# Kernel tuning notes

Measured on AMD Instinct MI355X. Metric: run time of the kernel, lower is better.

Reference implementation:

```python
import jax, jax.numpy as jnp
import numpy as np

N_NODES = 100000
N_EDGES = 1600000
IN_FEATS = 256
HIDDEN = 128
N_CLASSES = 128
NEG_SLOPE = 0.2


def setup_inputs() -> dict:
    key = jax.random.key(0)
    ks = jax.random.split(key, 12)
    inp = {
        "features": jax.random.normal(ks[0], (N_NODES, IN_FEATS), dtype=jnp.float32),
        "src": jax.random.randint(ks[1], (N_EDGES,), 0, N_NODES, dtype=jnp.int32),
        "dst": jax.random.randint(ks[2], (N_EDGES,), 0, N_NODES, dtype=jnp.int32),
        # layer 1 params (Xavier-ish scale)
        "W1": jax.random.normal(ks[3], (HIDDEN, IN_FEATS), dtype=jnp.float32) / np.sqrt(IN_FEATS),
        "al1": jax.random.normal(ks[4], (HIDDEN,), dtype=jnp.float32) / np.sqrt(HIDDEN),
        "ar1": jax.random.normal(ks[5], (HIDDEN,), dtype=jnp.float32) / np.sqrt(HIDDEN),
        "b1": jnp.zeros((HIDDEN,), dtype=jnp.float32),
        # layer 2 params
        "W2": jax.random.normal(ks[6], (N_CLASSES, HIDDEN), dtype=jnp.float32) / np.sqrt(HIDDEN),
        "al2": jax.random.normal(ks[7], (N_CLASSES,), dtype=jnp.float32) / np.sqrt(N_CLASSES),
        "ar2": jax.random.normal(ks[8], (N_CLASSES,), dtype=jnp.float32) / np.sqrt(N_CLASSES),
        "b2": jnp.zeros((N_CLASSES,), dtype=jnp.float32),
    }
    return inp


def _gat_conv(x, W, attn_l, attn_r, bias, src, dst):
    """Single-head DGL GATConv: fc -> edge leaky-relu scores -> segment softmax over dst -> scatter-sum."""
    h = x @ W.T                                   # [N, D]
    el = h @ attn_l                               # [N]
    er = h @ attn_r                               # [N]
    e = jax.nn.leaky_relu(el[src] + er[dst], NEG_SLOPE)   # [E]
    # numerically stable segment softmax over incoming edges of each dst node
    m = jax.ops.segment_max(e, dst, num_segments=N_NODES)          # [N] (-inf for empty)
    ex = jnp.exp(e - m[dst])                                       # [E]
    s = jax.ops.segment_sum(ex, dst, num_segments=N_NODES)         # [N]
    alpha = ex / s[dst]                                            # [E]
    out = jax.ops.segment_sum(h[src] * alpha[:, None], dst, num_segments=N_NODES)
    return out + bias


def reference(features, src, dst, W1, al1, ar1, b1, W2, al2, ar2, b2):
    x = _gat_conv(features, W1, al1, ar1, b1, src, dst)
    x = jax.nn.elu(x)
    return _gat_conv(x, W2, al2, ar2, b2, src, dst)
```

## Files before the change

kernel.cpp:

```cpp
#include <hip/hip_runtime.h>

typedef unsigned short u16;
typedef unsigned int u32;

#define NEG_SLOPE 0.2f

using short8 = __attribute__((ext_vector_type(8))) short;
using float4v = __attribute__((ext_vector_type(4))) float;

__device__ __forceinline__ float bfu(u16 v) { return __uint_as_float(((u32)v) << 16); }
__device__ __forceinline__ float bflo(u32 u) { return __uint_as_float(u << 16); }
__device__ __forceinline__ float bfhi(u32 u) { return __uint_as_float(u & 0xffff0000u); }
__device__ __forceinline__ u16 f2bf(float f) {
  u32 x = __float_as_uint(f);
  return (u16)((x + 0x7fffu + ((x >> 16) & 1u)) >> 16);
}
__device__ __forceinline__ float loadf(const void* p, int idx, int isbf) {
  return isbf ? bfu(((const u16*)p)[idx]) : ((const float*)p)[idx];
}

__global__ __launch_bounds__(256) void detect_dtype(const u32* __restrict__ w,
                                                    int nwords, int* __restrict__ flag) {
  __shared__ int cnt;
  if (threadIdx.x == 0) cnt = 0;
  __syncthreads();
  int c = 0;
  for (int i = threadIdx.x; i < nwords; i += 256) {
    u32 e = (w[i] >> 7) & 0xFFu;
    c += (e >= 0x60u && e <= 0x90u) ? 1 : 0;
  }
  atomicAdd(&cnt, c);
  __syncthreads();
  if (threadIdx.x == 0) flag[0] = (cnt * 2 > nwords) ? 1 : 0;
}

__global__ __launch_bounds__(256) void zero_i32(int* __restrict__ p, int n) {
  int i = blockIdx.x * 256 + threadIdx.x;
  if (i < n) p[i] = 0;
}


__global__ __launch_bounds__(256) void scan1(const int* __restrict__ counts,
                                             int* __restrict__ indptr,
                                             int* __restrict__ bsum, int N) {
  __shared__ int sh[256];
  int t = threadIdx.x;
  int idx = blockIdx.x * 256 + t;
  int v = (idx < N) ? counts[idx] : 0;
  sh[t] = v;
  __syncthreads();
  for (int off = 1; off < 256; off <<= 1) {
    int y = (t >= off) ? sh[t - off] : 0;
    __syncthreads();
    sh[t] += y;
    __syncthreads();
  }
  if (idx < N) indptr[idx] = sh[t] - v;
  if (t == 255) bsum[blockIdx.x] = sh[255];
}

__global__ __launch_bounds__(512) void scan2par(int* __restrict__ bsum, int NB) {
  __shared__ int sh[512];
  int t = threadIdx.x;
  int v = (t < NB) ? bsum[t] : 0;
  sh[t] = v;
  __syncthreads();
  for (int off = 1; off < 512; off <<= 1) {
    int y = (t >= off) ? sh[t - off] : 0;
    __syncthreads();
    sh[t] += y;
    __syncthreads();
  }
  if (t < NB) bsum[t] = sh[t] - v;
}

__global__ __launch_bounds__(256) void scan3(int* __restrict__ indptr,
                                             const int* __restrict__ boff,
                                             int N, int E) {
  int idx = blockIdx.x * 256 + threadIdx.x;
  if (idx < N) indptr[idx] += boff[blockIdx.x];
  if (idx == 0) indptr[N] = E;
}

__global__ __launch_bounds__(256) void scatter2(const int* __restrict__ src,
                                                const int* __restrict__ dst,
                                                const int* __restrict__ rank,
                                                const int* __restrict__ indptr,
                                                int* __restrict__ ssrc, int E) {
  int e = blockIdx.x * 256 + threadIdx.x;
  if (e < E) {
    int d = dst[e];
    ssrc[indptr[d] + rank[e]] = src[e];
  }
}

__global__ __launch_bounds__(256) void bsw_build(const void* __restrict__ W,
                                                 u16* __restrict__ Bsw, int K,
                                                 const int* __restrict__ dflag) {
  const int isbf = dflag[0];
  int t = blockIdx.x * 256 + threadIdx.x;
  int total = (K / 32) * 8 * 64;
  if (t >= total) return;
  int lane = t & 63;
  int c = (t >> 6) & 7;
  int ktile = t >> 9;
  int n = lane & 15, q = lane >> 4;
  int col = c * 16 + n;
  u16 vals[8];
#pragma unroll
  for (int j = 0; j < 8; ++j) {
    int k = ktile * 32 + q * 8 + j;
    int idx = col * K + k;
    vals[j] = isbf ? ((const u16*)W)[idx] : f2bf(((const float*)W)[idx]);
  }
  *(uint4*)(Bsw + (size_t)t * 8) = *(uint4*)vals;
}

template <int K, int DYNA>
__device__ __forceinline__ void gemm_body(int bix, const void* __restrict__ Xv,
                                          const u16* __restrict__ Bsw,
                                          u16* __restrict__ Hb,
                                          const void* __restrict__ al,
                                          const void* __restrict__ ar,
                                          float* __restrict__ el_,
                                          float* __restrict__ er_, int N,
                                          const int* __restrict__ dflag) {
  const int isbfP = dflag[0];
  const int isbfA = DYNA ? isbfP : 1;
  int tid = threadIdx.x;
  int w = tid >> 6, lane = tid & 63;
  int n = lane & 15, q = lane >> 4;
  int row0 = bix * 64 + w * 16;
  int m = row0 + n;
  int mclamp = (m < N) ? m : 0;

  float alv[8], arv[8];
#pragma unroll
  for (int c = 0; c < 8; ++c) {
    alv[c] = loadf(al, c * 16 + n, isbfP);
    arv[c] = loadf(ar, c * 16 + n, isbfP);
  }

  float4v acc[8];
#pragma unroll
  for (int c = 0; c < 8; ++c) acc[c] = (float4v){0.f, 0.f, 0.f, 0.f};

#pragma unroll
  for (int t = 0; t < K / 32; ++t) {
    short8 af;
    if (isbfA) {
      af = *(const short8*)((const u16*)Xv + (size_t)mclamp * K + t * 32 + q * 8);
    } else {
      const float* Af = (const float*)Xv + (size_t)mclamp * K + t * 32 + q * 8;
      float4 f0 = *(const float4*)Af;
      float4 f1 = *(const float4*)(Af + 4);
      u16 tmp[8] = {f2bf(f0.x), f2bf(f0.y), f2bf(f0.z), f2bf(f0.w),
                    f2bf(f1.x), f2bf(f1.y), f2bf(f1.z), f2bf(f1.w)};
      af = *(short8*)tmp;
    }
    const uint4* bt = (const uint4*)Bsw + ((size_t)t * 8) * 64 + lane;
#pragma unroll
    for (int c = 0; c < 8; ++c) {
      uint4 bw = bt[c * 64];
      short8 bf = *(short8*)&bw;
      acc[c] = __builtin_amdgcn_mfma_f32_16x16x32_bf16(af, bf, acc[c], 0, 0, 0);
    }
  }

#pragma unroll
  for (int c = 0; c < 8; ++c) {
#pragma unroll
    for (int r = 0; r < 4; ++r) {
      int row = row0 + q * 4 + r;
      if (row < N) Hb[(size_t)row * 128 + c * 16 + n] = f2bf(acc[c][r]);
    }
  }

#pragma unroll
  for (int r = 0; r < 4; ++r) {
    float sl = 0.f, sr = 0.f;
#pragma unroll
    for (int c = 0; c < 8; ++c) {
      float v = acc[c][r];
      sl = fmaf(v, alv[c], sl);
      sr = fmaf(v, arv[c], sr);
    }
#pragma unroll
    for (int off = 1; off < 16; off <<= 1) {
      sl += __shfl_xor(sl, off);
      sr += __shfl_xor(sr, off);
    }
    if (n == 0) {
      int row = row0 + q * 4 + r;
      if (row < N) {
        el_[row] = sl;
        er_[row] = sr;
      }
    }
  }
}

template <int K, int DYNA>
__global__ __launch_bounds__(256) void gemm_mfma(const void* __restrict__ Xv,
                                                 const u16* __restrict__ Bsw,
                                                 u16* __restrict__ Hb,
                                                 const void* __restrict__ al,
                                                 const void* __restrict__ ar,
                                                 float* __restrict__ el_,
                                                 float* __restrict__ er_, int N,
                                                 const int* __restrict__ dflag) {
  gemm_body<K, DYNA>(blockIdx.x, Xv, Bsw, Hb, al, ar, el_, er_, N, dflag);
}

template <int K, int DYNA>
__global__ __launch_bounds__(256) void fused_gemm_hist(
    const void* __restrict__ Xv, const u16* __restrict__ Bsw, u16* __restrict__ Hb,
    const void* __restrict__ al, const void* __restrict__ ar,
    float* __restrict__ el_, float* __restrict__ er_, int N,
    const int* __restrict__ dflag, int gemm_blocks,
    const int* __restrict__ dst, int* __restrict__ counts,
    int* __restrict__ rank, int E) {
  int bix = (int)blockIdx.x;
  if (bix < gemm_blocks) {
    gemm_body<K, DYNA>(bix, Xv, Bsw, Hb, al, ar, el_, er_, N, dflag);
  } else {
    int e = (bix - gemm_blocks) * 256 + threadIdx.x;
    if (e < E) rank[e] = atomicAdd(&counts[dst[e]], 1);
  }
}

template <int MODE>
__global__ __launch_bounds__(256) void agg_kernel(const u32* __restrict__ Hb,
                                                  const float* __restrict__ el,
                                                  const float* __restrict__ er,
                                                  const int* __restrict__ indptr,
                                                  const int* __restrict__ ssrc,
                                                  const void* __restrict__ bias,
                                                  void* __restrict__ outv, int N,
                                                  const int* __restrict__ dflag) {
  const int isbf = dflag[0];
  int tid = threadIdx.x;
  int n = blockIdx.x * 4 + (tid >> 6);
  int lane = tid & 63;
  if (n >= N) return;

  int beg = indptr[n];
  int end = indptr[n + 1];
  float ern = er[n];

  float ms[4], ll[4], aa0[4], aa1[4];
#pragma unroll
  for (int j = 0; j < 4; ++j) {
    ms[j] = -INFINITY; ll[j] = 0.f; aa0[j] = 0.f; aa1[j] = 0.f;
  }

  int p = beg;
  int id[8];
#pragma unroll
  for (int j = 0; j < 8; ++j) id[j] = (p + j < end) ? ssrc[p + j] : 0;
  float ev[4];
  u32 hv[4];
#pragma unroll
  for (int j = 0; j < 4; ++j) {
    ev[j] = el[id[j]];
    hv[j] = Hb[(size_t)id[j] * 64 + lane];
  }

  for (; p < end; p += 4) {
    float ev2[4];
    u32 hv2[4];
#pragma unroll
    for (int j = 0; j < 4; ++j) {
      ev2[j] = el[id[4 + j]];
      hv2[j] = Hb[(size_t)id[4 + j] * 64 + lane];
    }
    int idn[4];
#pragma unroll
    for (int j = 0; j < 4; ++j) idn[j] = (p + 8 + j < end) ? ssrc[p + 8 + j] : 0;

#pragma unroll
    for (int j = 0; j < 4; ++j) {
      if (p + j < end) {
        float sc = ev[j] + ern;
        sc = (sc > 0.f) ? sc : NEG_SLOPE * sc;
        float mn = fmaxf(ms[j], sc);
        float corr = __expf(ms[j] - mn), pe = __expf(sc - mn);
        ll[j] = ll[j] * corr + pe;
        aa0[j] = aa0[j] * corr + pe * bflo(hv[j]);
        aa1[j] = aa1[j] * corr + pe * bfhi(hv[j]);
        ms[j] = mn;
      }
    }
#pragma unroll
    for (int j = 0; j < 4; ++j) {
      id[j] = id[4 + j];
      id[4 + j] = idn[j];
      ev[j] = ev2[j];
      hv[j] = hv2[j];
    }
  }

  float mm = fmaxf(fmaxf(ms[0], ms[1]), fmaxf(ms[2], ms[3]));
  float msafe = (mm > -INFINITY) ? mm : 0.f;
  float l = 0.f, a0 = 0.f, a1 = 0.f;
#pragma unroll
  for (int j = 0; j < 4; ++j) {
    float c = __expf(ms[j] - msafe);
    l += ll[j] * c;
    a0 += aa0[j] * c;
    a1 += aa1[j] * c;
  }
  float inv = (l > 0.f) ? 1.f / l : 0.f;
  float o0 = a0 * inv + loadf(bias, 2 * lane, isbf);
  float o1 = a1 * inv + loadf(bias, 2 * lane + 1, isbf);

  if (MODE == 0) {
    o0 = (o0 > 0.f) ? o0 : (__expf(o0) - 1.f);
    o1 = (o1 > 0.f) ? o1 : (__expf(o1) - 1.f);
    ((u32*)outv)[(size_t)n * 64 + lane] = (u32)f2bf(o0) | ((u32)f2bf(o1) << 16);
  } else {
    if (isbf) {
      ((u32*)outv)[(size_t)n * 64 + lane] = (u32)f2bf(o0) | ((u32)f2bf(o1) << 16);
    } else {
      ((float2*)outv)[(size_t)n * 64 + lane] = make_float2(o0, o1);
    }
  }
}


extern "C" void kernel_launch(void* const* d_in, const int* in_sizes, int n_in,
                              void* d_out, int out_size, void* d_ws, size_t ws_size,
                              hipStream_t stream) {
  const int IN_FEATS = 256, HID = 128;
  const void* features = d_in[0];
  const int* src = (const int*)d_in[1];
  const int* dst = (const int*)d_in[2];
  const void* W1 = d_in[3];
  const void* al1 = d_in[4];
  const void* ar1 = d_in[5];
  const void* b1 = d_in[6];
  const void* W2 = d_in[7];
  const void* al2 = d_in[8];
  const void* ar2 = d_in[9];
  const void* b2 = d_in[10];

  const int N = in_sizes[0] / IN_FEATS;
  const int E = in_sizes[1];

  char* p = (char*)d_ws;
  auto alloc = [&](size_t bytes) -> void* {
    void* q = (void*)p;
    p += (bytes + 255) & ~(size_t)255;
    return q;
  };
  int* dflag = (int*)alloc(256);
  u16* Bsw1 = (u16*)alloc((size_t)(IN_FEATS / 32) * 8 * 64 * 8 * 2);
  u16* Bsw2 = (u16*)alloc((size_t)(HID / 32) * 8 * 64 * 8 * 2);
  u16* hb = (u16*)alloc((size_t)N * HID * 2);
  u16* x = (u16*)alloc((size_t)N * HID * 2);
  float* el = (float*)alloc((size_t)N * 4);
  float* er = (float*)alloc((size_t)N * 4);
  int* counts = (int*)alloc((size_t)N * 4);
  int* indptr = (int*)alloc((size_t)(N + 1) * 4);
  int* rank = (int*)alloc((size_t)E * 4);
  int* bsum = (int*)alloc((size_t)((N + 255) / 256) * 4);
  int* ssrc = (int*)alloc((size_t)E * 4);

  const int NB = (N + 255) / 256;
  const int EB = (E + 255) / 256;
  const int GEMM_B = (N + 63) / 64;
  const int NODE_B = (N + 3) / 4;

  detect_dtype<<<1, 256, 0, stream>>>((const u32*)features, 4096, dflag);
  zero_i32<<<NB, 256, 0, stream>>>(counts, N);
  bsw_build<<<((IN_FEATS / 32) * 8 * 64 + 255) / 256, 256, 0, stream>>>(W1, Bsw1, IN_FEATS, dflag);
  bsw_build<<<((HID / 32) * 8 * 64 + 255) / 256, 256, 0, stream>>>(W2, Bsw2, HID, dflag);

  fused_gemm_hist<IN_FEATS, 1><<<GEMM_B + EB, 256, 0, stream>>>(
      features, Bsw1, hb, al1, ar1, el, er, N, dflag, GEMM_B, dst, counts, rank, E);

  scan1<<<NB, 256, 0, stream>>>(counts, indptr, bsum, N);
  scan2par<<<1, 512, 0, stream>>>(bsum, NB);
  scan3<<<NB, 256, 0, stream>>>(indptr, bsum, N, E);
  scatter2<<<EB, 256, 0, stream>>>(src, dst, rank, indptr, ssrc, E);

  agg_kernel<0><<<NODE_B, 256, 0, stream>>>((const u32*)hb, el, er, indptr, ssrc, b1, (void*)x, N, dflag);

  gemm_mfma<HID, 0><<<GEMM_B, 256, 0, stream>>>((const void*)x, Bsw2, hb, al2, ar2, el, er, N, dflag);
  agg_kernel<1><<<NODE_B, 256, 0, stream>>>((const u32*)hb, el, er, indptr, ssrc, b2, d_out, N, dflag);
}
```

Before: 518.8 us.

## Replicate degree histogram per XCC and stage GEMM output through LDS

The in-degree histogram is split into eight copies, one per XCC, chosen from the hardware XCC id. Atomics use workgroup scope so they can resolve in the local L2 rather than going device-wide. Each rank packs the replica index in its top bits, and the scan and scatter kernels now fold per-replica prefix offsets into indptr and the edge placement. Separately, the GEMM writes its bf16 tile to padded shared memory and stores it to global as coalesced 16-byte rows instead of scattered 2-byte stores. The risks are the larger zero-fill and scan read of 8N counters, and relying on workgroup-scope atomics being coherent among all blocks on one XCC.

New measurement: 537.5 us. 1.04x slower.

```diff
diff --git a/kernel.cpp b/kernel.cpp
--- a/kernel.cpp
+++ b/kernel.cpp
@@ -17,6 +17,16 @@
 }
 __device__ __forceinline__ float loadf(const void* p, int idx, int isbf) {
   return isbf ? bfu(((const u16*)p)[idx]) : ((const float*)p)[idx];
+}
+
+__device__ __forceinline__ int xcc_id() {
+  unsigned v;
+  asm volatile("s_getreg_b32 %0, hwreg(20, 0, 8)" : "=s"(v));
+  return (int)(v & 7u);
+}
+
+__device__ __forceinline__ int l2_atomic_add(int* p) {
+  return __hip_atomic_fetch_add(p, 1, __ATOMIC_RELAXED, __HIP_MEMORY_SCOPE_WORKGROUP);
 }
 
 __global__ __launch_bounds__(256) void detect_dtype(const u32* __restrict__ w,
@@ -40,13 +50,23 @@
 }
 
 
-__global__ __launch_bounds__(256) void scan1(const int* __restrict__ counts,
+__global__ __launch_bounds__(256) void scan1(int* __restrict__ cnt8,
                                              int* __restrict__ indptr,
                                              int* __restrict__ bsum, int N) {
   __shared__ int sh[256];
   int t = threadIdx.x;
   int idx = blockIdx.x * 256 + t;
-  int v = (idx < N) ? counts[idx] : 0;
+  int v = 0;
+  if (idx < N) {
+    int s = 0;
+#pragma unroll
+    for (int r = 0; r < 8; ++r) {
+      int c = cnt8[r * N + idx];
+      cnt8[r * N + idx] = s;
+      s += c;
+    }
+    v = s;
+  }
   sh[t] = v;
   __syncthreads();
   for (int off = 1; off < 256; off <<= 1) {
@@ -86,11 +106,15 @@
                                                 const int* __restrict__ dst,
                                                 const int* __restrict__ rank,
                                                 const int* __restrict__ indptr,
-                                                int* __restrict__ ssrc, int E) {
+                                                const int* __restrict__ cnt8,
+                                                int* __restrict__ ssrc, int E, int N) {
   int e = blockIdx.x * 256 + threadIdx.x;
   if (e < E) {
     int d = dst[e];
-    ssrc[indptr[d] + rank[e]] = src[e];
+    u32 rk = (u32)rank[e];
+    int rep = (int)(rk >> 28);
+    int lr = (int)(rk & 0x0FFFFFFFu);
+    ssrc[indptr[d] + cnt8[rep * N + d] + lr] = src[e];
   }
 }
 
@@ -116,6 +140,8 @@
   *(uint4*)(Bsw + (size_t)t * 8) = *(uint4*)vals;
 }
 
+#define ST_PAD 136
+
 template <int K, int DYNA>
 __device__ __forceinline__ void gemm_body(int bix, const void* __restrict__ Xv,
                                           const u16* __restrict__ Bsw,
@@ -124,7 +150,8 @@
                                           const void* __restrict__ ar,
                                           float* __restrict__ el_,
                                           float* __restrict__ er_, int N,
-                                          const int* __restrict__ dflag) {
+                                          const int* __restrict__ dflag,
+                                          u16* __restrict__ st) {
   const int isbfP = dflag[0];
   const int isbfA = DYNA ? isbfP : 1;
   int tid = threadIdx.x;
@@ -167,12 +194,21 @@
     }
   }
 
+  u16* stw = st + w * (16 * ST_PAD);
 #pragma unroll
   for (int c = 0; c < 8; ++c) {
 #pragma unroll
     for (int r = 0; r < 4; ++r) {
-      int row = row0 + q * 4 + r;
-      if (row < N) Hb[(size_t)row * 128 + c * 16 + n] = f2bf(acc[c][r]);
+      stw[(q * 4 + r) * ST_PAD + c * 16 + n] = f2bf(acc[c][r]);
+    }
+  }
+#pragma unroll
+  for (int pass = 0; pass < 4; ++pass) {
+    int row = pass * 4 + q;
+    int gr = row0 + row;
+    if (gr < N) {
+      uint4 v = *(const uint4*)(stw + row * ST_PAD + n * 8);
+      *(uint4*)(Hb + (size_t)gr * 128 + n * 8) = v;
     }
   }
 
@@ -209,7 +245,8 @@
                                                  float* __restrict__ el_,
                                                  float* __restrict__ er_, int N,
                                                  const int* __restrict__ dflag) {
-  gemm_body<K, DYNA>(blockIdx.x, Xv, Bsw, Hb, al, ar, el_, er_, N, dflag);
+  __shared__ u16 st[4 * 16 * ST_PAD];
+  gemm_body<K, DYNA>(blockIdx.x, Xv, Bsw, Hb, al, ar, el_, er_, N, dflag, st);
 }
 
 template <int K, int DYNA>
@@ -218,14 +255,30 @@
     const void* __restrict__ al, const void* __restrict__ ar,
     float* __restrict__ el_, float* __restrict__ er_, int N,
     const int* __restrict__ dflag, int gemm_blocks,
-    const int* __restrict__ dst, int* __restrict__ counts,
+    const int* __restrict__ dst, int* __restrict__ cnt8,
     int* __restrict__ rank, int E) {
+  __shared__ u16 st[4 * 16 * ST_PAD];
   int bix = (int)blockIdx.x;
   if (bix < gemm_blocks) {
-    gemm_body<K, DYNA>(bix, Xv, Bsw, Hb, al, ar, el_, er_, N, dflag);
+    gemm_body<K, DYNA>(bix, Xv, Bsw, Hb, al, ar, el_, er_, N, dflag, st);
   } else {
-    int e = (bix - gemm_blocks) * 256 + threadIdx.x;
-    if (e < E) rank[e] = atomicAdd(&counts[dst[e]], 1);
+    int base = (bix - gemm_blocks) * 1024 + (int)threadIdx.x * 4;
+    int rep = xcc_id();
+    int* cbase = cnt8 + rep * N;
+    int rt = rep << 28;
+    if (base + 3 < E) {
+      int4 dv = *(const int4*)(dst + base);
+      int r0 = l2_atomic_add(&cbase[dv.x]);
+      int r1 = l2_atomic_add(&cbase[dv.y]);
+      int r2 = l2_atomic_add(&cbase[dv.z]);
+      int r3 = l2_atomic_add(&cbase[dv.w]);
+      *(int4*)(rank + base) = make_int4(r0 | rt, r1 | rt, r2 | rt, r3 | rt);
+    } else {
+      for (int j = 0; j < 4; ++j) {
+        int e = base + j;
+        if (e < E) rank[e] = rt | l2_atomic_add(&cbase[dst[e]]);
+      }
+    }
   }
 }
 
@@ -360,7 +413,7 @@
   u16* x = (u16*)alloc((size_t)N * HID * 2);
   float* el = (float*)alloc((size_t)N * 4);
   float* er = (float*)alloc((size_t)N * 4);
-  int* counts = (int*)alloc((size_t)N * 4);
+  int* cnt8 = (int*)alloc((size_t)8 * N * 4);
   int* indptr = (int*)alloc((size_t)(N + 1) * 4);
   int* rank = (int*)alloc((size_t)E * 4);
   int* bsum = (int*)alloc((size_t)((N + 255) / 256) * 4);
@@ -368,21 +421,22 @@
 
   const int NB = (N + 255) / 256;
   const int EB = (E + 255) / 256;
+  const int HEB = (E + 1023) / 1024;
   const int GEMM_B = (N + 63) / 64;
   const int NODE_B = (N + 3) / 4;
 
   detect_dtype<<<1, 256, 0, stream>>>((const u32*)features, 4096, dflag);
-  zero_i32<<<NB, 256, 0, stream>>>(counts, N);
+  zero_i32<<<(8 * N + 255) / 256, 256, 0, stream>>>(cnt8, 8 * N);
   bsw_build<<<((IN_FEATS / 32) * 8 * 64 + 255) / 256, 256, 0, stream>>>(W1, Bsw1, IN_FEATS, dflag);
   bsw_build<<<((HID / 32) * 8 * 64 + 255) / 256, 256, 0, stream>>>(W2, Bsw2, HID, dflag);
 
-  fused_gemm_hist<IN_FEATS, 1><<<GEMM_B + EB, 256, 0, stream>>>(
-      features, Bsw1, hb, al1, ar1, el, er, N, dflag, GEMM_B, dst, counts, rank, E);
-
-  scan1<<<NB, 256, 0, stream>>>(counts, indptr, bsum, N);
+  fused_gemm_hist<IN_FEATS, 1><<<GEMM_B + HEB, 256, 0, stream>>>(
+      features, Bsw1, hb, al1, ar1, el, er, N, dflag, GEMM_B, dst, cnt8, rank, E);
+
+  scan1<<<NB, 256, 0, stream>>>(cnt8, indptr, bsum, N);
   scan2par<<<1, 512, 0, stream>>>(bsum, NB);
   scan3<<<NB, 256, 0, stream>>>(indptr, bsum, N, E);
-  scatter2<<<EB, 256, 0, stream>>>(src, dst, rank, indptr, ssrc, E);
+  scatter2<<<EB, 256, 0, stream>>>(src, dst, rank, indptr, cnt8, ssrc, E, N);
 
   agg_kernel<0><<<NODE_B, 256, 0, stream>>>((const u32*)hb, el, er, indptr, ssrc, b1, (void*)x, N, dflag);
 
```
